# Performance work log

Measured on AMD Instinct MI355X. Metric: run time of the kernel, lower is better.

The kernel has to match this reference:

```python
import jax, jax.numpy as jnp
import numpy as np

D_MODEL = 256      # num_nodes == d_model (forced by pre_relation mask shape)
MW = 2             # moving_window (hardcoded '2' in MPNN reshape)
STRIDE = 1
DECAY = 0.7
INPUT_DIM = 64
OUTPUT_DIM = 64
BN_EPS = 1e-5


def _mask_matrix():
    # Mask_Matrix: block (i,j) of size d_model x d_model equals decay**|i-j|
    blocks = DECAY ** np.abs(np.arange(MW)[:, None] - np.arange(MW)[None, :])
    return jnp.asarray(np.kron(blocks, np.ones((D_MODEL, D_MODEL))).astype(np.float32))


def _bn(h, w, b):
    # training-mode BatchNorm1d over channel-last layout [B, N, C]
    mu = h.mean(axis=(0, 1))
    var = h.var(axis=(0, 1))  # biased variance, as torch uses for normalization
    return (h - mu) * jax.lax.rsqrt(var + BN_EPS) * w + b


def setup_inputs() -> dict:
    key = jax.random.key(0)
    ks = jax.random.split(key, 4)
    bs, scale_num = 16, 17
    x = jax.random.normal(ks[0], (bs, scale_num, D_MODEL, INPUT_DIM), jnp.float32)
    # mapping2 weights scaled small to keep the dot-product softmax well conditioned
    w_map2 = jax.random.normal(ks[1], (INPUT_DIM, INPUT_DIM), jnp.float32) * 0.05
    b_map2 = jnp.zeros((INPUT_DIM,), jnp.float32)
    bn0_w = jnp.ones((INPUT_DIM,), jnp.float32)
    bn0_b = jnp.zeros((INPUT_DIM,), jnp.float32)
    th0_w = jax.random.normal(ks[2], (OUTPUT_DIM, INPUT_DIM), jnp.float32) / np.float32(np.sqrt(INPUT_DIM))
    th0_b = jnp.zeros((OUTPUT_DIM,), jnp.float32)
    th1_w = jax.random.normal(ks[3], (OUTPUT_DIM, INPUT_DIM), jnp.float32) / np.float32(np.sqrt(INPUT_DIM))
    th1_b = jnp.zeros((OUTPUT_DIM,), jnp.float32)
    bn1_w = jnp.ones((OUTPUT_DIM,), jnp.float32)
    bn1_b = jnp.zeros((OUTPUT_DIM,), jnp.float32)
    return dict(x=x, w_map2=w_map2, b_map2=b_map2, bn0_w=bn0_w, bn0_b=bn0_b,
                th0_w=th0_w, th0_b=th0_b, th1_w=th1_w, th1_b=th1_b,
                bn1_w=bn1_w, bn1_b=bn1_b)


def reference(x, w_map2, b_map2, bn0_w, bn0_b, th0_w, th0_b, th1_w, th1_b, bn1_w, bn1_b):
    bs, S, N, F = x.shape
    L = (S - MW) // STRIDE + 1  # num_windows from F.unfold
    # WindowConv_Graph + transpose(2,3) + reshape: X[b,l,m,n,f] = x[b, l*stride+m, n, f]
    idx = np.arange(L)[:, None] * STRIDE + np.arange(MW)[None, :]
    X = x[:, idx].reshape(bs * L, MW * N, F)  # [B', N1, F]

    # Dot_Graph_Construction_weights (N1 != d_model -> mapping2 branch)
    nf = X @ w_map2.T + b_map2                       # [B', N1, F]
    adj = jnp.einsum('bnf,bmf->bnm', nf, nf)         # [B', N1, N1]
    eye = jnp.eye(MW * N, dtype=x.dtype)
    adj = jax.nn.leaky_relu(adj - eye * 1e8)
    adj = jax.nn.softmax(adj, axis=-1) + eye

    # decay mask multiply
    adj = adj * _mask_matrix()

    # BatchNorm over input_dim channels
    xb = _bn(nf, bn0_w, bn0_b)

    # MPNN_mk_v2, field=2, way='sum'
    out = (adj @ xb) @ th0_w.T + th0_b               # hop 1
    adj2 = adj @ adj
    out = out + (adj2 @ xb) @ th1_w.T + th1_b        # hop 2
    out = jax.nn.leaky_relu(_bn(out, bn1_w, bn1_b))

    # pooling over the moving_window axis (mean), then over windows (mean)
    out = out.reshape(bs, L, MW, N, OUTPUT_DIM).mean(axis=2)
    return out.mean(axis=1)  # [bs, num_nodes, output_dim]
```

## Files before the change

### kernel.cpp

```cpp
#include <hip/hip_runtime.h>


typedef unsigned short u16;
typedef __bf16 bf16x8 __attribute__((ext_vector_type(8)));
typedef float f32x4 __attribute__((ext_vector_type(4)));
typedef unsigned int u32x4 __attribute__((ext_vector_type(4)));

#define MFMA16(a, b, c) __builtin_amdgcn_mfma_f32_16x16x32_bf16(a, b, c, 0, 0, 0)

#define BSZ 16
#define SNUM 17
#define FD 64
#define NB 256
#define N1 512
#define SL_ELEMS 16384
#define Y_ELEMS (BSZ * SNUM * SL_ELEMS)

#define WM_O 0
#define BM_O 4096
#define B0W_O 4160
#define B0B_O 4224
#define T0W_O 4288
#define T0B_O 8384
#define T1W_O 8448
#define T1B_O 12544
#define B1W_O 12608
#define B1B_O 12672
#define P_TOT 12736

#define SLAB2_O 32768
#define RED_O 65536
#define SCR_O 65792
#define LDS_U16 (SCR_O + 8 * 640)

__device__ __forceinline__ float bf2f(u16 u) {
    union { unsigned int i; float f; } v;
    v.i = ((unsigned int)u) << 16;
    return v.f;
}
__device__ __forceinline__ u16 f2bu(float f) {
    __bf16 h = (__bf16)f;
    return __builtin_bit_cast(u16, h);
}
__device__ __forceinline__ u16 f2bf(float f) {
    unsigned int u = __builtin_bit_cast(unsigned int, f);
    unsigned int r = (u + 0x7fffu + ((u >> 16) & 1u)) >> 16;
    return (u16)r;
}
__device__ __forceinline__ bf16x8 ld8g(const u16* p) {
    return __builtin_bit_cast(bf16x8, *reinterpret_cast<const u32x4*>(p));
}

__global__ __launch_bounds__(256) void k_prep(
    const void* p0, const void* p1, const void* p2, const void* p3,
    const void* p4, const void* p5, const void* p6, const void* p7,
    const void* p8, const void* p9, int* __restrict__ flagOut,
    u16* __restrict__ pc, float* __restrict__ stats) {
    const int tid = threadIdx.x, lane = tid & 63;
    int z = 0, bc = 0;
    const unsigned int* w = (const unsigned int*)p0;
    for (int i = lane; i < 2048; i += 64) {
        const unsigned int v = w[i];
        z += ((v & 0xffffu) == 0u);
        bc += (v >> 14) & 1;
    }
#pragma unroll
    for (int o = 1; o < 64; o <<= 1) {
        z += __shfl_xor(z, o);
        bc += __shfl_xor(bc, o);
    }
    const int flag = (z > 1024 || bc > 256) ? 1 : 0;
    if (blockIdx.x == 0) {
        if (tid == 0) *flagOut = flag;
        if (tid < 256) stats[tid] = 0.f;
    }
    const int i = blockIdx.x * 256 + tid;
    if (i >= P_TOT) return;
    const void* src;
    int si;
    if (i < BM_O)        { src = p0; si = i; }
    else if (i < B0W_O)  { src = p1; si = i - BM_O; }
    else if (i < B0B_O)  { src = p2; si = i - B0W_O; }
    else if (i < T0W_O)  { src = p3; si = i - B0B_O; }
    else if (i < T0B_O)  { src = p4; si = i - T0W_O; }
    else if (i < T1W_O)  { src = p5; si = i - T0B_O; }
    else if (i < T1B_O)  { src = p6; si = i - T1W_O; }
    else if (i < B1W_O)  { src = p7; si = i - T1B_O; }
    else if (i < B1B_O)  { src = p8; si = i - B1W_O; }
    else                 { src = p9; si = i - B1B_O; }
    pc[i] = flag ? f2bf(((const float*)src)[si]) : ((const u16*)src)[si];
}

__global__ __launch_bounds__(256) void k_y(const void* __restrict__ xv,
                                           const int* __restrict__ flag,
                                           const u16* __restrict__ pc,
                                           u16* __restrict__ y,
                                           float* __restrict__ gstats) {
    const int slice = blockIdx.x;
    const int tid = threadIdx.x, wave = tid >> 6, lane = tid & 63;
    const int quad = lane >> 4, l16 = lane & 15;
    __shared__ float red[128];
    if (tid < 128) red[tid] = 0.f;
    const int isf32 = *flag;

    f32x4 acc[4][4];
#pragma unroll
    for (int i = 0; i < 4; i++)
#pragma unroll
        for (int j = 0; j < 4; j++) acc[i][j] = (f32x4){0.f, 0.f, 0.f, 0.f};

    bf16x8 bfr[4][2];
#pragma unroll
    for (int nt = 0; nt < 4; nt++)
#pragma unroll
        for (int kh = 0; kh < 2; kh++)
            bfr[nt][kh] = ld8g(pc + WM_O + (nt * 16 + l16) * 64 + kh * 32 + quad * 8);

    const float* xf = (const float*)xv + (size_t)slice * SL_ELEMS;
    const u16* xh = (const u16*)xv + (size_t)slice * SL_ELEMS;

#pragma unroll
    for (int mt = 0; mt < 4; mt++) {
        const int row = wave * 64 + mt * 16 + l16;
        bf16x8 a0, a1;
        if (isf32) {
            const float* r0 = xf + row * 64 + quad * 8;
            f32x4 v0 = *(const f32x4*)r0;
            f32x4 v1 = *(const f32x4*)(r0 + 4);
            f32x4 v2 = *(const f32x4*)(r0 + 32);
            f32x4 v3 = *(const f32x4*)(r0 + 36);
#pragma unroll
            for (int j = 0; j < 4; j++) {
                a0[j] = (__bf16)v0[j]; a0[4 + j] = (__bf16)v1[j];
                a1[j] = (__bf16)v2[j]; a1[4 + j] = (__bf16)v3[j];
            }
        } else {
            a0 = ld8g(xh + row * 64 + quad * 8);
            a1 = ld8g(xh + row * 64 + 32 + quad * 8);
        }
#pragma unroll
        for (int nt = 0; nt < 4; nt++)
            acc[mt][nt] = MFMA16(a1, bfr[nt][1], MFMA16(a0, bfr[nt][0], acc[mt][nt]));
    }

    u16* ys = y + (size_t)slice * SL_ELEMS;
    float s1[4] = {0.f, 0.f, 0.f, 0.f}, s2[4] = {0.f, 0.f, 0.f, 0.f};
#pragma unroll
    for (int nt = 0; nt < 4; nt++) {
        const int col = nt * 16 + l16;
        const float bias = bf2f(pc[BM_O + col]);
#pragma unroll
        for (int mt = 0; mt < 4; mt++)
#pragma unroll
            for (int r = 0; r < 4; r++) {
                const int row = wave * 64 + mt * 16 + quad * 4 + r;
                const float v = acc[mt][nt][r] + bias;
                ys[row * 64 + col] = f2bu(v);
                s1[nt] += v;
                s2[nt] += v * v;
            }
        s1[nt] += __shfl_xor(s1[nt], 16); s1[nt] += __shfl_xor(s1[nt], 32);
        s2[nt] += __shfl_xor(s2[nt], 16); s2[nt] += __shfl_xor(s2[nt], 32);
    }
    __syncthreads();
    if (quad == 0) {
#pragma unroll
        for (int nt = 0; nt < 4; nt++) {
            atomicAdd(&red[nt * 16 + l16], s1[nt]);
            atomicAdd(&red[64 + nt * 16 + l16], s2[nt]);
        }
    }
    __syncthreads();
    const int s = slice % SNUM;
    const float wgt = (s == 0 || s == SNUM - 1) ? 1.f : 2.f;
    if (tid < 128) atomicAdd(&gstats[tid], red[tid] * wgt);
}

__device__ __forceinline__ void stage_slab1(u16* slab1, const u16* ybase,
                                            int tid) {
#pragma unroll
    for (int i = 0; i < 8; i++) {
        const int gid = i * 512 + tid, n = gid >> 3, g = gid & 7;
        *(u32x4*)(slab1 + n * 64 + ((g ^ (n & 7)) << 3)) =
            *(const u32x4*)(ybase + n * 64 + g * 8);
    }
}

__global__ __launch_bounds__(512)
__attribute__((amdgpu_waves_per_eu(2, 2)))
void k_h1(const u16* __restrict__ y, const float* __restrict__ stats,
          const u16* __restrict__ pc, u16* __restrict__ z1g) {
    __shared__ u16 lds[LDS_U16];
    u16* slab1 = lds;
    u16* slab2 = lds + SLAB2_O;
    const int tid = threadIdx.x, w = tid >> 6, lane = tid & 63;
    const int quad = lane >> 4, l16 = lane & 15;
    u16* scr = lds + SCR_O + w * 640;
    const int g = blockIdx.x, p = g >> 1, half = g & 1;
    const int b = p >> 4, l = p & 15;
    const f32x4 ZERO4 = (f32x4){0.f, 0.f, 0.f, 0.f};

    const float cinv = 1.f / 131072.f;
    const int fme = tid & 63;
    float mu0 = stats[fme] * cinv;
    float vr0 = fmaxf(stats[64 + fme] * cinv - mu0 * mu0, 0.f);
    const float scale_f = rsqrtf(vr0 + 1e-5f) * bf2f(pc[B0W_O + fme]);
    const float shift_f = bf2f(pc[B0B_O + fme]) - mu0 * scale_f;

    const u16* ybase = y + (size_t)(b * SNUM + l) * SL_ELEMS;
    stage_slab1(slab1, ybase, tid);
    __syncthreads();

#pragma unroll
    for (int i = 0; i < 8; i++) {
        const int gn = w + i * 8;
        union { u16 u[8]; u32x4 v; } pk;
#pragma unroll
        for (int j = 0; j < 8; j++) {
            const int n = gn * 8 + j;
            const u16 raw = slab1[n * 64 + (((fme >> 3) ^ (n & 7)) << 3) + (fme & 7)];
            pk.u[j] = f2bu(bf2f(raw) * scale_f + shift_f);
        }
        *(u32x4*)(slab2 + fme * 512 + ((gn ^ fme) << 3)) = pk.v;
    }
    __syncthreads();

    bf16x8 a[2][2];
#pragma unroll
    for (int st = 0; st < 2; st++)
#pragma unroll
        for (int h = 0; h < 2; h++) {
            const int row = half * 256 + w * 32 + st * 16 + l16;
            a[st][h] = *(const bf16x8*)(slab1 + row * 64 + (((h * 4 + quad) ^ (row & 7)) << 3));
        }

    const float mb = (half == 0) ? 0.7f : (1.0f / 0.7f);
    const float me = (half == 0) ? (1.0f / 0.7f) : 1.0f;

    f32x4 oacc[2][4];
    f32x4 lsum[2];
#pragma unroll
    for (int st = 0; st < 2; st++) {
        lsum[st] = ZERO4;
#pragma unroll
        for (int ft = 0; ft < 4; ft++) oacc[st][ft] = ZERO4;
    }

#pragma unroll 1
    for (int c = 0; c < 8; c++) {
        if (c == 4) {
#pragma unroll
            for (int st = 0; st < 2; st++)
#pragma unroll
                for (int r = 0; r < 4; r++) lsum[st][r] *= mb;
        }
        const float lmf = ((half == 1) == (c >= 4)) ? 0.f : -0.5145731728f;
#pragma unroll
        for (int ch = 0; ch < 2; ch++) {
            const int colbase = c * 64 + ch * 32;
            f32x4 S[2][2];
#pragma unroll
            for (int jt = 0; jt < 2; jt++) {
                const int rj = colbase + jt * 16 + l16;
                const bf16x8 b0 = *(const bf16x8*)(slab1 + rj * 64 + ((quad ^ (rj & 7)) << 3));
                const bf16x8 b1 = *(const bf16x8*)(slab1 + rj * 64 + (((4 + quad) ^ (rj & 7)) << 3));
#pragma unroll
                for (int st = 0; st < 2; st++)
                    S[st][jt] = MFMA16(a[st][1], b1, MFMA16(a[st][0], b0, ZERO4));
            }
            bf16x8 pa[2];
#pragma unroll
            for (int st = 0; st < 2; st++) {
                const int rowbase = half * 256 + w * 32 + st * 16;
#pragma unroll
                for (int jt = 0; jt < 2; jt++)
#pragma unroll
                    for (int r = 0; r < 4; r++) {
                        const float s = S[st][jt][r];
                        const float m2 = s > 0.f ? 1.44269504f : 0.0144269504f;
                        float pv = exp2f(fminf(fmaf(s, m2, lmf), 86.f));
                        if (colbase + jt * 16 == rowbase && l16 == quad * 4 + r) pv = 0.f;
                        lsum[st][r] += pv;
                        scr[(quad * 4 + r) * 40 + jt * 16 + l16] = f2bu(pv);
                    }
                pa[st] = *(const bf16x8*)(scr + l16 * 40 + quad * 8);
            }
#pragma unroll
            for (int ft = 0; ft < 4; ft++) {
                const int f = ft * 16 + l16, gn = c * 8 + ch * 4 + quad;
                const bf16x8 bv = *(const bf16x8*)(slab2 + f * 512 + ((gn ^ f) << 3));
                oacc[0][ft] = MFMA16(pa[0], bv, oacc[0][ft]);
                oacc[1][ft] = MFMA16(pa[1], bv, oacc[1][ft]);
            }
        }
    }
#pragma unroll
    for (int st = 0; st < 2; st++)
#pragma unroll
        for (int r = 0; r < 4; r++) {
            lsum[st][r] += __shfl_xor(lsum[st][r], 1);
            lsum[st][r] += __shfl_xor(lsum[st][r], 2);
            lsum[st][r] += __shfl_xor(lsum[st][r], 4);
            lsum[st][r] += __shfl_xor(lsum[st][r], 8);
        }

#pragma unroll
    for (int st = 0; st < 2; st++) {
        f32x4 inv;
#pragma unroll
        for (int r = 0; r < 4; r++) inv[r] = __builtin_amdgcn_rcpf(lsum[st][r] * me);
#pragma unroll
        for (int ft = 0; ft < 4; ft++)
#pragma unroll
            for (int r = 0; r < 4; r++) {
                const int i = half * 256 + w * 32 + st * 16 + quad * 4 + r;
                const int f = ft * 16 + l16;
                const float xbv = bf2f(slab2[f * 512 + (((i >> 3) ^ f) << 3) + (i & 7)]);
                z1g[(size_t)p * (N1 * FD) + (size_t)i * 64 + f] =
                    f2bu(oacc[st][ft][r] * inv[r] + xbv);
            }
    }
}

__global__ __launch_bounds__(512)
__attribute__((amdgpu_waves_per_eu(2, 2)))
void k_h2(const u16* __restrict__ y, const u16* __restrict__ z1g,
          float* __restrict__ stats, const u16* __restrict__ pc,
          u16* __restrict__ opre) {
    __shared__ u16 lds[LDS_U16];
    u16* slab1 = lds;
    u16* slab2 = lds + SLAB2_O;
    float* red = (float*)(lds + RED_O);
    const int tid = threadIdx.x, w = tid >> 6, lane = tid & 63;
    const int quad = lane >> 4, l16 = lane & 15;
    u16* scr = lds + SCR_O + w * 640;
    const int g = blockIdx.x, p = g >> 1, half = g & 1;
    const int b = p >> 4, l = p & 15;
    const f32x4 ZERO4 = (f32x4){0.f, 0.f, 0.f, 0.f};
    const int fme = tid & 63;

    if (tid < 128) red[tid] = 0.f;

    const u16* ybase = y + (size_t)(b * SNUM + l) * SL_ELEMS;
    stage_slab1(slab1, ybase, tid);

    const u16* zbase = z1g + (size_t)p * (N1 * FD);
#pragma unroll
    for (int i = 0; i < 8; i++) {
        const int gn = w + i * 8;
        union { u16 u[8]; u32x4 v; } pk;
#pragma unroll
        for (int j = 0; j < 8; j++) {
            const int n = gn * 8 + j;
            pk.u[j] = zbase[n * 64 + fme];
        }
        *(u32x4*)(slab2 + fme * 512 + ((gn ^ fme) << 3)) = pk.v;
    }
    __syncthreads();

    bf16x8 a[2][2];
#pragma unroll
    for (int st = 0; st < 2; st++)
#pragma unroll
        for (int h = 0; h < 2; h++) {
            const int row = half * 256 + w * 32 + st * 16 + l16;
            a[st][h] = *(const bf16x8*)(slab1 + row * 64 + (((h * 4 + quad) ^ (row & 7)) << 3));
        }

    const float mb = (half == 0) ? 0.7f : (1.0f / 0.7f);
    const float me = (half == 0) ? (1.0f / 0.7f) : 1.0f;

    f32x4 oacc[2][4];
    f32x4 lsum[2];
#pragma unroll
    for (int st = 0; st < 2; st++) {
        lsum[st] = ZERO4;
#pragma unroll
        for (int ft = 0; ft < 4; ft++) oacc[st][ft] = ZERO4;
    }

#pragma unroll 1
    for (int c = 0; c < 8; c++) {
        if (c == 4) {
#pragma unroll
            for (int st = 0; st < 2; st++)
#pragma unroll
                for (int r = 0; r < 4; r++) lsum[st][r] *= mb;
        }
        const float lmf = ((half == 1) == (c >= 4)) ? 0.f : -0.5145731728f;
#pragma unroll
        for (int ch = 0; ch < 2; ch++) {
            const int colbase = c * 64 + ch * 32;
            f32x4 S[2][2];
#pragma unroll
            for (int jt = 0; jt < 2; jt++) {
                const int rj = colbase + jt * 16 + l16;
                const bf16x8 b0 = *(const bf16x8*)(slab1 + rj * 64 + ((quad ^ (rj & 7)) << 3));
                const bf16x8 b1 = *(const bf16x8*)(slab1 + rj * 64 + (((4 + quad) ^ (rj & 7)) << 3));
#pragma unroll
                for (int st = 0; st < 2; st++)
                    S[st][jt] = MFMA16(a[st][1], b1, MFMA16(a[st][0], b0, ZERO4));
            }
            bf16x8 pa[2];
#pragma unroll
            for (int st = 0; st < 2; st++) {
                const int rowbase = half * 256 + w * 32 + st * 16;
#pragma unroll
                for (int jt = 0; jt < 2; jt++)
#pragma unroll
                    for (int r = 0; r < 4; r++) {
                        const float s = S[st][jt][r];
                        const float m2 = s > 0.f ? 1.44269504f : 0.0144269504f;
                        float pv = exp2f(fminf(fmaf(s, m2, lmf), 86.f));
                        if (colbase + jt * 16 == rowbase && l16 == quad * 4 + r) pv = 0.f;
                        lsum[st][r] += pv;
                        scr[(quad * 4 + r) * 40 + jt * 16 + l16] = f2bu(pv);
                    }
                pa[st] = *(const bf16x8*)(scr + l16 * 40 + quad * 8);
            }
#pragma unroll
            for (int ft = 0; ft < 4; ft++) {
                const int f = ft * 16 + l16, gn = c * 8 + ch * 4 + quad;
                const bf16x8 bv = *(const bf16x8*)(slab2 + f * 512 + ((gn ^ f) << 3));
                oacc[0][ft] = MFMA16(pa[0], bv, oacc[0][ft]);
                oacc[1][ft] = MFMA16(pa[1], bv, oacc[1][ft]);
            }
        }
    }
#pragma unroll
    for (int st = 0; st < 2; st++)
#pragma unroll
        for (int r = 0; r < 4; r++) {
            lsum[st][r] += __shfl_xor(lsum[st][r], 1);
            lsum[st][r] += __shfl_xor(lsum[st][r], 2);
            lsum[st][r] += __shfl_xor(lsum[st][r], 4);
            lsum[st][r] += __shfl_xor(lsum[st][r], 8);
        }

    float s1a[4] = {0.f, 0.f, 0.f, 0.f}, s2a[4] = {0.f, 0.f, 0.f, 0.f};
#pragma unroll
    for (int st = 0; st < 2; st++) {
        f32x4 inv;
#pragma unroll
        for (int r = 0; r < 4; r++) inv[r] = __builtin_amdgcn_rcpf(lsum[st][r] * me);
#pragma unroll
        for (int ft = 0; ft < 4; ft++)
#pragma unroll
            for (int r = 0; r < 4; r++) {
                const int i = half * 256 + w * 32 + st * 16 + quad * 4 + r;
                const int f = ft * 16 + l16;
                const float o1 = bf2f(slab2[f * 512 + (((i >> 3) ^ f) << 3) + (i & 7)]);
                oacc[st][ft][r] = oacc[st][ft][r] * inv[r] + o1;
            }
        bf16x8 a1[2], a2[2];
        const int irow = half * 256 + w * 32 + st * 16 + l16;
#pragma unroll
        for (int h = 0; h < 2; h++)
#pragma unroll
            for (int j = 0; j < 8; j++) {
                const int f = h * 32 + quad * 8 + j;
                const u16 raw = slab2[f * 512 + (((irow >> 3) ^ f) << 3) + (irow & 7)];
                a1[h][j] = __builtin_bit_cast(__bf16, raw);
            }
#pragma unroll
        for (int h = 0; h < 2; h++) {
#pragma unroll
            for (int ftl = 0; ftl < 2; ftl++)
#pragma unroll
                for (int r = 0; r < 4; r++)
                    scr[(quad * 4 + r) * 40 + ftl * 16 + l16] = f2bu(oacc[st][2 * h + ftl][r]);
            a2[h] = *(const bf16x8*)(scr + l16 * 40 + quad * 8);
        }
        f32x4 pacc[4];
#pragma unroll
        for (int ot = 0; ot < 4; ot++) {
            const int o = ot * 16 + l16;
            const float bias = bf2f(pc[T0B_O + o]) + bf2f(pc[T1B_O + o]);
            pacc[ot] = (f32x4){bias, bias, bias, bias};
        }
#pragma unroll
        for (int h = 0; h < 2; h++)
#pragma unroll
            for (int ot = 0; ot < 4; ot++) {
                const int o = ot * 16 + l16;
                bf16x8 w0f = ld8g(pc + T0W_O + o * 64 + h * 32 + quad * 8);
                bf16x8 w1f = ld8g(pc + T1W_O + o * 64 + h * 32 + quad * 8);
                pacc[ot] = MFMA16(a1[h], w0f, pacc[ot]);
                pacc[ot] = MFMA16(a2[h], w1f, pacc[ot]);
            }
#pragma unroll
        for (int ot = 0; ot < 4; ot++)
#pragma unroll
            for (int r = 0; r < 4; r++) {
                const int i = half * 256 + w * 32 + st * 16 + quad * 4 + r;
                const int o = ot * 16 + l16;
                const float v = pacc[ot][r];
                s1a[ot] += v;
                s2a[ot] += v * v;
                opre[(size_t)p * (N1 * FD) + (size_t)i * 64 + o] = f2bu(v);
            }
    }
#pragma unroll
    for (int ot = 0; ot < 4; ot++) {
        s1a[ot] += __shfl_xor(s1a[ot], 16); s1a[ot] += __shfl_xor(s1a[ot], 32);
        s2a[ot] += __shfl_xor(s2a[ot], 16); s2a[ot] += __shfl_xor(s2a[ot], 32);
    }
    if (quad == 0) {
#pragma unroll
        for (int ot = 0; ot < 4; ot++) {
            atomicAdd(&red[ot * 16 + l16], s1a[ot]);
            atomicAdd(&red[64 + ot * 16 + l16], s2a[ot]);
        }
    }
    __syncthreads();
    if (tid < 128) atomicAdd(&stats[128 + tid], red[tid]);
}

__global__ __launch_bounds__(256) void k_final(const u16* __restrict__ op,
                                               const float* __restrict__ stats,
                                               const u16* __restrict__ pc,
                                               float* __restrict__ out) {
    const int o = blockIdx.x * 256 + threadIdx.x;
    const int f = o & 63, n = (o >> 6) & 255, b = o >> 14;
    const float inv = 1.f / 131072.f;
    const float mu = stats[128 + f] * inv;
    const float var = fmaxf(stats[192 + f] * inv - mu * mu, 0.f);
    const float rs = rsqrtf(var + 1e-5f);
    const float scale = rs * bf2f(pc[B1W_O + f]);
    const float shift = bf2f(pc[B1B_O + f]) - mu * scale;
    float acc = 0.f;
    for (int l = 0; l < 16; l++) {
        const size_t pb = (size_t)(b * 16 + l) * N1 * FD;
#pragma unroll
        for (int m = 0; m < 2; m++) {
            float v = bf2f(op[pb + (size_t)(m * 256 + n) * 64 + f]);
            v = v * scale + shift;
            acc += (v > 0.f ? v : 0.01f * v);
        }
    }
    out[o] = acc * (1.f / 32.f);
}

extern "C" void kernel_launch(void* const* d_in, const int* in_sizes, int n_in,
                              void* d_out, int out_size, void* d_ws, size_t ws_size,
                              hipStream_t stream) {
    char* ws = (char*)d_ws;
    size_t off = 0;
    auto alloc = [&](size_t bytes) { void* pp = ws + off; off += (bytes + 255) & ~(size_t)255; return pp; };
    u16* y = (u16*)alloc((size_t)Y_ELEMS * 2);
    u16* z1 = (u16*)alloc((size_t)NB * N1 * FD * 2);
    u16* opre = (u16*)alloc((size_t)NB * N1 * FD * 2);
    u16* pc = (u16*)alloc(P_TOT * 2);
    float* stats = (float*)alloc(256 * 4);
    int* flag = (int*)alloc(256);
    float* out = (float*)d_out;

    k_prep<<<50, 256, 0, stream>>>(d_in[1], d_in[2], d_in[3], d_in[4], d_in[5],
                                   d_in[6], d_in[7], d_in[8], d_in[9], d_in[10],
                                   flag, pc, stats);
    k_y<<<BSZ * SNUM, 256, 0, stream>>>(d_in[0], flag, pc, y, stats);
    k_h1<<<2 * NB, 512, 0, stream>>>(y, stats, pc, z1);
    k_h2<<<2 * NB, 512, 0, stream>>>(y, z1, stats, pc, opre);
    k_final<<<1024, 256, 0, stream>>>(opre, stats, pc, out);
}
```

Measured before the change: 213.7 us.

## Store hop-1 result as pre-swizzled LDS image and fully unroll column loops

k_h1 now writes its hop-1 output through LDS into a transposed, XOR-swizzled layout that matches what k_h2 needs in its slab2. Each half-block writes its own 256-row portion with 16-byte vector stores. k_h2 can then fill slab2 with plain contiguous 16-byte copies instead of gathering scalar u16 elements with stride 64. Both kernels also fully unroll the 8-iteration column loop, which may raise register pressure under the fixed waves-per-EU constraint.

```diff
diff --git a/kernel.cpp b/kernel.cpp
--- a/kernel.cpp
+++ b/kernel.cpp
@@ -189,7 +189,7 @@
 __global__ __launch_bounds__(512)
 __attribute__((amdgpu_waves_per_eu(2, 2)))
 void k_h1(const u16* __restrict__ y, const float* __restrict__ stats,
-          const u16* __restrict__ pc, u16* __restrict__ z1g) {
+          const u16* __restrict__ pc, u16* __restrict__ z1img) {
     __shared__ u16 lds[LDS_U16];
     u16* slab1 = lds;
     u16* slab2 = lds + SLAB2_O;
@@ -246,7 +246,7 @@
         for (int ft = 0; ft < 4; ft++) oacc[st][ft] = ZERO4;
     }
 
-#pragma unroll 1
+#pragma unroll
     for (int c = 0; c < 8; c++) {
         if (c == 4) {
 #pragma unroll
@@ -316,15 +316,35 @@
                 const int i = half * 256 + w * 32 + st * 16 + quad * 4 + r;
                 const int f = ft * 16 + l16;
                 const float xbv = bf2f(slab2[f * 512 + (((i >> 3) ^ f) << 3) + (i & 7)]);
-                z1g[(size_t)p * (N1 * FD) + (size_t)i * 64 + f] =
-                    f2bu(oacc[st][ft][r] * inv[r] + xbv);
-            }
+                oacc[st][ft][r] = oacc[st][ft][r] * inv[r] + xbv;
+            }
+    }
+    __syncthreads();
+#pragma unroll
+    for (int st = 0; st < 2; st++)
+#pragma unroll
+        for (int ft = 0; ft < 4; ft++)
+#pragma unroll
+            for (int r = 0; r < 4; r++) {
+                const int i = half * 256 + w * 32 + st * 16 + quad * 4 + r;
+                const int f = ft * 16 + l16;
+                slab2[f * 512 + (((i >> 3) ^ f) << 3) + (i & 7)] = f2bu(oacc[st][ft][r]);
+            }
+    __syncthreads();
+    {
+        const int fr = tid >> 3, seg = tid & 7;
+        const int off = (((half * 32) ^ (fr & 32)) << 3) + seg * 32;
+        u16* dst = z1img + (size_t)p * 32768 + fr * 512 + off;
+        const u16* srcp = slab2 + fr * 512 + off;
+#pragma unroll
+        for (int k = 0; k < 4; k++)
+            *(u32x4*)(dst + k * 8) = *(const u32x4*)(srcp + k * 8);
     }
 }
 
 __global__ __launch_bounds__(512)
 __attribute__((amdgpu_waves_per_eu(2, 2)))
-void k_h2(const u16* __restrict__ y, const u16* __restrict__ z1g,
+void k_h2(const u16* __restrict__ y, const u16* __restrict__ z1img,
           float* __restrict__ stats, const u16* __restrict__ pc,
           u16* __restrict__ opre) {
     __shared__ u16 lds[LDS_U16];
@@ -337,24 +357,17 @@
     const int g = blockIdx.x, p = g >> 1, half = g & 1;
     const int b = p >> 4, l = p & 15;
     const f32x4 ZERO4 = (f32x4){0.f, 0.f, 0.f, 0.f};
-    const int fme = tid & 63;
 
     if (tid < 128) red[tid] = 0.f;
 
     const u16* ybase = y + (size_t)(b * SNUM + l) * SL_ELEMS;
     stage_slab1(slab1, ybase, tid);
 
-    const u16* zbase = z1g + (size_t)p * (N1 * FD);
+    const u16* zsrc = z1img + (size_t)p * 32768;
 #pragma unroll
     for (int i = 0; i < 8; i++) {
-        const int gn = w + i * 8;
-        union { u16 u[8]; u32x4 v; } pk;
-#pragma unroll
-        for (int j = 0; j < 8; j++) {
-            const int n = gn * 8 + j;
-            pk.u[j] = zbase[n * 64 + fme];
-        }
-        *(u32x4*)(slab2 + fme * 512 + ((gn ^ fme) << 3)) = pk.v;
+        const int gid = i * 512 + tid;
+        *(u32x4*)(slab2 + gid * 8) = *(const u32x4*)(zsrc + gid * 8);
     }
     __syncthreads();
 
@@ -379,7 +392,7 @@
         for (int ft = 0; ft < 4; ft++) oacc[st][ft] = ZERO4;
     }
 
-#pragma unroll 1
+#pragma unroll
     for (int c = 0; c < 8; c++) {
         if (c == 4) {
 #pragma unroll
@@ -548,7 +561,7 @@
     size_t off = 0;
     auto alloc = [&](size_t bytes) { void* pp = ws + off; off += (bytes + 255) & ~(size_t)255; return pp; };
     u16* y = (u16*)alloc((size_t)Y_ELEMS * 2);
-    u16* z1 = (u16*)alloc((size_t)NB * N1 * FD * 2);
+    u16* z1img = (u16*)alloc((size_t)NB * 32768 * 2);
     u16* opre = (u16*)alloc((size_t)NB * N1 * FD * 2);
     u16* pc = (u16*)alloc(P_TOT * 2);
     float* stats = (float*)alloc(256 * 4);
@@ -559,7 +572,7 @@
                                    d_in[6], d_in[7], d_in[8], d_in[9], d_in[10],
                                    flag, pc, stats);
     k_y<<<BSZ * SNUM, 256, 0, stream>>>(d_in[0], flag, pc, y, stats);
-    k_h1<<<2 * NB, 512, 0, stream>>>(y, stats, pc, z1);
-    k_h2<<<2 * NB, 512, 0, stream>>>(y, z1, stats, pc, opre);
+    k_h1<<<2 * NB, 512, 0, stream>>>(y, stats, pc, z1img);
+    k_h2<<<2 * NB, 512, 0, stream>>>(y, z1img, stats, pc, opre);
     k_final<<<1024, 256, 0, stream>>>(opre, stats, pc, out);
 }
```

Measured after the change: 248.6 us. +16.4%, slower.
